# Kernel optimization log

Hardware: AMD Instinct MI355X
Metric: run time of the kernel (lower is better)

## Reference

```python
import jax, jax.numpy as jnp
import numpy as np

NUM_HEADS = 16

def setup_inputs() -> dict:
    key = jax.random.key(0)
    ks = jax.random.split(key, 5)
    N, T, D = 16, 4096, 1024
    # Linear weights stored as (in, out): y = x @ W + b (equivalent to torch x @ W.T + b)
    return {
        "x": jax.random.normal(ks[0], (N, T, D), jnp.float32),
        "w_qkv": jax.random.normal(ks[1], (D, 3 * D), jnp.float32) * (D ** -0.5),
        "b_qkv": jax.random.normal(ks[2], (3 * D,), jnp.float32) * 0.02,
        "w_proj": jax.random.normal(ks[3], (D, D), jnp.float32) * (D ** -0.5),
        "b_proj": jax.random.normal(ks[4], (D,), jnp.float32) * 0.02,
    }

def reference(x, w_qkv, b_qkv, w_proj, b_proj):
    N, T, D = x.shape
    H = NUM_HEADS
    hd = D // H
    scale = hd ** -0.5
    qkv = x @ w_qkv + b_qkv                      # (N,T,3D)
    qkv = qkv.reshape(N, T, 3, H, hd)
    q, k, v = qkv[:, :, 0], qkv[:, :, 1], qkv[:, :, 2]   # each (N,T,H,hd)
    # Faithful to source: matmul over last two dims -> scores across HEADS, (N,T,H,H)
    attn = jnp.einsum('nthd,ntgd->nthg', q * scale, k)
    attn = jax.nn.softmax(attn, axis=-1)
    out = jnp.einsum('nthg,ntgd->nthd', attn, v)         # (N,T,H,hd)
    # Faithful: transpose(2,1) then flatten -> (N,H,T,hd).reshape(N,T,D)
    out = out.transpose(0, 2, 1, 3).reshape(N, T, D)
    return out @ w_proj + b_proj
```

## Files before the change

kernel.cpp:

```cpp
#include <hip/hip_runtime.h>
#include <hip/hip_bf16.h>
#include <stdint.h>

typedef __bf16 bf16x8 __attribute__((ext_vector_type(8)));
typedef float f32x4 __attribute__((ext_vector_type(4)));
typedef unsigned short us8 __attribute__((ext_vector_type(8)));

__device__ __forceinline__ float bf2f(unsigned short u) {
    return __uint_as_float(((unsigned)u) << 16);
}
__device__ __forceinline__ unsigned short f2bf(float f) {
    __bf16 b = (__bf16)f;
    return __builtin_bit_cast(unsigned short, b);
}

__device__ __forceinline__ void gload16(const char* g, char* l) {
    __builtin_amdgcn_global_load_lds(
        (const __attribute__((address_space(1))) void*)g,
        (__attribute__((address_space(3))) void*)l, 16, 0, 0);
}

__global__ __launch_bounds__(256) void transpose_cast(
    const float* __restrict__ in, unsigned short* __restrict__ out,
    int K, int N)
{
    __shared__ float tile[32][33];
    const int tx = threadIdx.x, ty = threadIdx.y;
    const int n0 = blockIdx.x * 32, k0 = blockIdx.y * 32;
    #pragma unroll
    for (int i = 0; i < 32; i += 8)
        tile[ty + i][tx] = in[(long)(k0 + ty + i) * N + n0 + tx];
    __syncthreads();
    #pragma unroll
    for (int i = 0; i < 32; i += 8)
        out[(long)(n0 + ty + i) * K + k0 + tx] = f2bf(tile[tx][ty + i]);
}

__global__ __launch_bounds__(256) void cast_f32_bf16(
    const float* __restrict__ in, unsigned short* __restrict__ out, long n)
{
    const long stride = (long)gridDim.x * 256 * 8;
    for (long i = ((long)blockIdx.x * 256 + threadIdx.x) * 8; i < n; i += stride) {
        const f32x4 u0 = *(const f32x4*)&in[i];
        const f32x4 u1 = *(const f32x4*)&in[i + 4];
        us8 w;
        #pragma unroll
        for (int e = 0; e < 4; ++e) { w[e] = f2bf(u0[e]); w[e + 4] = f2bf(u1[e]); }
        *(us8*)&out[i] = w;
    }
}

#define MFMA16x16(a, b, c) __builtin_amdgcn_mfma_f32_16x16x32_bf16(a, b, c, 0, 0, 0)
#define BAR __builtin_amdgcn_s_barrier()
#define SB  __builtin_amdgcn_sched_barrier(0)
#define P1_ __builtin_amdgcn_s_setprio(1);
#define P0_ __builtin_amdgcn_s_setprio(0);

#define MFMA_H(AA, BB, RO, CO)                                                 \
    _Pragma("unroll") for (int mi_ = 0; mi_ < 4; ++mi_)                        \
        _Pragma("unroll") for (int ni_ = 0; ni_ < 2; ++ni_)                    \
            acc[(RO)+mi_][(CO)+ni_] =                                          \
                MFMA16x16(AA[mi_], BB[ni_], acc[(RO)+mi_][(CO)+ni_]);

#define RD_A(DST, BUFOFF, HIOFF, KS)                                           \
    _Pragma("unroll") for (int mi_ = 0; mi_ < 4; ++mi_)                        \
        DST[mi_] = *(const bf16x8*)(smem + (BUFOFF) + aBase + (HIOFF) + mi_*2048 + (KS));

#define RD_B(DST, BUFOFF, NOFF, KS)                                            \
    _Pragma("unroll") for (int ni_ = 0; ni_ < 2; ++ni_)                        \
        DST[ni_] = *(const bf16x8*)(smem + (BUFOFF) + bBase + ((NOFF)+ni_)*2048 + (KS));

#define TILE8(T_, BUF, OBUF, SG, SR)                                           \
  do {                                                                         \
    const long gk = (long)((T_) + 2) * 128;                                    \
                                                 \
    RD_A(AH0, BUF, 8192, k0)                                                   \
    SB; asm volatile("s_waitcnt lgkmcnt(4)"); SB;                              \
    P1_ MFMA_H(AL0, BL0, 0, 0) P0_                                             \
                                                 \
    RD_B(BH0, BUF, 2, k0)                                                      \
    SB; asm volatile("s_waitcnt lgkmcnt(2)"); SB;                              \
    P1_ MFMA_H(AH0, BL0, 4, 0) P0_                                             \
                                                 \
    RD_A(AL1, BUF, 0, k1)                                                      \
    SB; asm volatile("s_waitcnt lgkmcnt(4)"); SB;                              \
    P1_ MFMA_H(AH0, BH0, 4, 2) P0_                                             \
                                  \
    BAR; RD_B(BL1, BUF, 0, k1)                                                 \
    if (SG) {                                                                  \
        gload16(aStage + (long)(0*64)*Kb + gk, smem + (BUF) + 0*8192 + ldsW);  \
        gload16(aStage + (long)(2*64)*Kb + gk, smem + (BUF) + 2*8192 + ldsW);  \
    }                                                                          \
    SB; asm volatile("s_waitcnt lgkmcnt(2)"); SB;                              \
    P1_ MFMA_H(AL0, BH0, 0, 2) P0_                                             \
                                                 \
    RD_A(AH1, BUF, 8192, k1)                                                   \
    SB; asm volatile("s_waitcnt lgkmcnt(4)"); SB;                              \
    P1_ MFMA_H(AL1, BL1, 0, 0) P0_                                             \
                   \
    BAR; RD_B(BH1, BUF, 2, k1)                                                 \
    if (SG) {                                                                  \
        gload16(aStage + (long)(1*64)*Kb + gk, smem + (BUF) + 1*8192 + ldsW);  \
        gload16(aStage + (long)(3*64)*Kb + gk, smem + (BUF) + 3*8192 + ldsW);  \
    }                                                                          \
    SB; asm volatile("s_waitcnt lgkmcnt(2)"); SB;                              \
    P1_ MFMA_H(AH1, BL1, 4, 0) P0_                                             \
    SB;                                                                        \
    if (SG) asm volatile("s_waitcnt vmcnt(4)");                                \
    else    asm volatile("s_waitcnt vmcnt(0)");                                \
    SB;                                                                        \
                           \
    BAR;                                                                       \
    if (SR) { RD_B(BL0, OBUF, 0, k0) }                                         \
    if (SG) {                                                                  \
        gload16(bStage + (long)(0*64)*Kb + gk, smem + (BUF) + 32768 + 0*8192 + ldsW); \
        gload16(bStage + (long)(1*64)*Kb + gk, smem + (BUF) + 32768 + 1*8192 + ldsW); \
    }                                                                          \
    SB;                                                                        \
    if (SR) asm volatile("s_waitcnt lgkmcnt(2)");                              \
    else    asm volatile("s_waitcnt lgkmcnt(0)");                              \
    SB;                                                                        \
    P1_ MFMA_H(AH1, BH1, 4, 2) P0_                                             \
                           \
    BAR;                                                                       \
    if (SR) { RD_A(AL0, OBUF, 0, k0) }                                         \
    if (SG) {                                                                  \
        gload16(bStage + (long)(2*64)*Kb + gk, smem + (BUF) + 32768 + 2*8192 + ldsW); \
        gload16(bStage + (long)(3*64)*Kb + gk, smem + (BUF) + 32768 + 3*8192 + ldsW); \
    }                                                                          \
    SB;                                                                        \
    if (SR) asm volatile("s_waitcnt lgkmcnt(4)");                              \
    else    asm volatile("s_waitcnt lgkmcnt(0)");                              \
    SB;                                                                        \
    P1_ MFMA_H(AL1, BH1, 0, 2) P0_                                             \
  } while (0)

template<bool OUT_BF16>
__global__ __launch_bounds__(512, 2)
void gemm256(const unsigned short* __restrict__ A,
             const unsigned short* __restrict__ BT,
             const float* __restrict__ bias,
             void* __restrict__ Cp,
             int M, int N, int K)
{
    extern __shared__ char smem[];
    const int tid  = threadIdx.x;
    const int lane = tid & 63;
    const int w    = tid >> 6;
    const int wm   = w >> 2;
    const int wn   = w & 3;

    const int nwg  = gridDim.x;
    const int bid0 = blockIdx.x;
    const int bid  = (bid0 & 7) * (nwg >> 3) + (bid0 >> 3);
    const int nbx  = N >> 8;
    const int bx   = bid % nbx, by = bid / nbx;
    const long rowStart = (long)by * 256;
    const int  colStart = bx * 256;

    const long Kb = (long)K * 2;

    const int srow = w * 8 + (lane >> 3);
    const int scol = ((lane & 7) ^ (lane >> 3)) << 4;
    const char* aStage = (const char*)A  + (rowStart + srow) * Kb + scol;
    const char* bStage = (const char*)BT + ((long)colStart + srow) * Kb + scol;
    const int ldsW = w * 1024;

    const int fr = lane & 15;
    const int kq = lane >> 4;
    const int sw = (fr & 7) << 4;
    const int k0 = (kq * 16) ^ sw;
    const int k1 = (64 + kq * 16) ^ sw;
    const int aBase = (wm * 128 + fr) * 128;
    const int bBase = 32768 + (wn * 64 + fr) * 128;

    f32x4 acc[8][4] = {};
    bf16x8 AL0[4], AH0[4], AL1[4], AH1[4], BL0[2], BH0[2], BL1[2], BH1[2];

    #pragma unroll
    for (int tt = 0; tt < 2; ++tt) {
        #pragma unroll
        for (int j = 0; j < 4; ++j)
            gload16(aStage + (long)(j * 64) * Kb + (long)tt * 128,
                    smem + tt * 65536 + j * 8192 + ldsW);
        #pragma unroll
        for (int j = 0; j < 4; ++j)
            gload16(bStage + (long)(j * 64) * Kb + (long)tt * 128,
                    smem + tt * 65536 + 32768 + j * 8192 + ldsW);
    }
    asm volatile("s_waitcnt vmcnt(8)");
    BAR;
    RD_B(BL0, 0, 0, k0)
    RD_A(AL0, 0, 0, k0)

    #pragma unroll 1
    for (int tp = 0; tp < 7; ++tp) {
        TILE8(2 * tp,     0,     65536, 1, 1);
        TILE8(2 * tp + 1, 65536, 0,     1, 1);
    }
    TILE8(14, 0,     65536, 0, 1);
    TILE8(15, 65536, 0,     0, 0);

    float bv[4];
    #pragma unroll
    for (int ni = 0; ni < 4; ++ni)
        bv[ni] = bias[colStart + wn * 64 + ni * 16 + fr];
    #pragma unroll
    for (int mi = 0; mi < 8; ++mi) {
        #pragma unroll
        for (int ni = 0; ni < 4; ++ni) {
            const int col = colStart + wn * 64 + ni * 16 + fr;
            #pragma unroll
            for (int e = 0; e < 4; ++e) {
                const long row = rowStart + wm * 128 + mi * 16 + kq * 4 + e;
                const float val = acc[mi][ni][e] + bv[ni];
                if constexpr (OUT_BF16)
                    ((unsigned short*)Cp)[row * N + col] = f2bf(val);
                else
                    ((float*)Cp)[row * N + col] = val;
            }
        }
    }
}

__global__ __launch_bounds__(256) void attn_kernel(
    const unsigned short* __restrict__ qkv, unsigned short* __restrict__ out)
{
    __shared__ unsigned short qkvs[4][3072];
    __shared__ float ps[4][320];
    __shared__ unsigned short os[4][1024];
    const int tid = threadIdx.x, lane = tid & 63, wave = tid >> 6;
    const long blockTok = (long)blockIdx.x * 4;

    const unsigned short* src = qkv + blockTok * 3072;
    unsigned short* dstBase = &qkvs[0][0];
    #pragma unroll
    for (int i = 0; i < 6; ++i) {
        const int o = (i * 256 + tid) * 8;
        *(us8*)&dstBase[o] = *(const us8*)&src[o];
    }
    __syncthreads();

    const unsigned short* q  = &qkvs[wave][0];
    const unsigned short* kk = &qkvs[wave][1024];
    const unsigned short* vv = &qkvs[wave][2048];

    const int fr = lane & 15, kq = lane >> 4;
    const int fo = fr * 64 + kq * 8;
    const bf16x8 aq0 = *(const bf16x8*)&q[fo];
    const bf16x8 aq1 = *(const bf16x8*)&q[fo + 32];
    const bf16x8 bk0 = *(const bf16x8*)&kk[fo];
    const bf16x8 bk1 = *(const bf16x8*)&kk[fo + 32];
    f32x4 s = {};
    s = __builtin_amdgcn_mfma_f32_16x16x32_bf16(aq0, bk0, s, 0, 0, 0);
    s = __builtin_amdgcn_mfma_f32_16x16x32_bf16(aq1, bk1, s, 0, 0, 0);

    #pragma unroll
    for (int r = 0; r < 4; ++r) {
        const float v_ = s[r] * 0.125f;
        float m_ = v_;
        m_ = fmaxf(m_, __shfl_xor(m_, 1, 64));
        m_ = fmaxf(m_, __shfl_xor(m_, 2, 64));
        m_ = fmaxf(m_, __shfl_xor(m_, 4, 64));
        m_ = fmaxf(m_, __shfl_xor(m_, 8, 64));
        const float p_ = expf(v_ - m_);
        float t_ = p_;
        t_ += __shfl_xor(t_, 1, 64);
        t_ += __shfl_xor(t_, 2, 64);
        t_ += __shfl_xor(t_, 4, 64);
        t_ += __shfl_xor(t_, 8, 64);
        ps[wave][(kq * 4 + r) * 20 + fr] = p_ / t_;
    }
    __syncthreads();

    const int h = lane >> 2, db = lane & 3;
    float o16[16] = {};
    #pragma unroll
    for (int gq = 0; gq < 4; ++gq) {
        const f32x4 pv = *(const f32x4*)&ps[wave][h * 20 + gq * 4];
        #pragma unroll
        for (int j = 0; j < 4; ++j) {
            const float pg = pv[j];
            const int g = gq * 4 + j;
            const us8 v8a = *(const us8*)&vv[g * 64 + db * 16];
            const us8 v8b = *(const us8*)&vv[g * 64 + db * 16 + 8];
            #pragma unroll
            for (int e = 0; e < 8; ++e) {
                o16[e]     += pg * bf2f(v8a[e]);
                o16[8 + e] += pg * bf2f(v8b[e]);
            }
        }
    }
    us8 w0, w1;
    #pragma unroll
    for (int e = 0; e < 8; ++e) { w0[e] = f2bf(o16[e]); w1[e] = f2bf(o16[8 + e]); }
    *(us8*)&os[wave][h * 64 + db * 16] = w0;
    *(us8*)&os[wave][h * 64 + db * 16 + 8] = w1;
    __syncthreads();

    #pragma unroll
    for (int i = 0; i < 2; ++i) {
        const int c = i * 256 + tid;
        const int w2 = c >> 7;
        const int cc = c & 127;
        const long m = blockTok + w2;
        const long n_ = m >> 12;
        const int t = (int)(m & 4095);
        const int hh = cc >> 3, slot = cc & 7;
        const long row = n_ * 4096 + hh * 256 + (t >> 4);
        const long colb = (long)(t & 15) * 128 + slot * 16;
        *(us8*)((char*)out + row * 2048 + colb) = *(const us8*)&os[w2][cc * 8];
    }
}

extern "C" void kernel_launch(void* const* d_in, const int* in_sizes, int n_in,
                              void* d_out, int out_size, void* d_ws, size_t ws_size,
                              hipStream_t stream) {
    const float* x      = (const float*)d_in[0];
    const float* w_qkv  = (const float*)d_in[1];
    const float* b_qkv  = (const float*)d_in[2];
    const float* w_proj = (const float*)d_in[3];
    const float* b_proj = (const float*)d_in[4];

    const long M = 65536;
    const size_t QKV_B = (size_t)M * 3072 * 2;
    const size_t XB_B  = (size_t)M * 1024 * 2;
    const size_t WQ_B  = 3072 * 1024 * 2;
    const size_t WP_B  = 1024 * 1024 * 2;
    if (ws_size < QKV_B + XB_B + WQ_B + WP_B) return;

    char* ws = (char*)d_ws;
    unsigned short* qkv    = (unsigned short*)ws;
    unsigned short* xb     = (unsigned short*)(ws + QKV_B);
    unsigned short* wqkvT  = (unsigned short*)(ws + QKV_B + XB_B);
    unsigned short* wprojT = (unsigned short*)(ws + QKV_B + XB_B + WQ_B);

    hipFuncSetAttribute((const void*)gemm256<true>,
                        hipFuncAttributeMaxDynamicSharedMemorySize, 131072);
    hipFuncSetAttribute((const void*)gemm256<false>,
                        hipFuncAttributeMaxDynamicSharedMemorySize, 131072);

    dim3 tb(32, 8);
    transpose_cast<<<dim3(3072 / 32, 1024 / 32), tb, 0, stream>>>(w_qkv, wqkvT, 1024, 3072);
    transpose_cast<<<dim3(1024 / 32, 1024 / 32), tb, 0, stream>>>(w_proj, wprojT, 1024, 1024);
    cast_f32_bf16<<<2048, 256, 0, stream>>>(x, xb, M * 1024);

    gemm256<true><<<dim3((3072 / 256) * (M / 256)), 512, 131072, stream>>>(
        xb, wqkvT, b_qkv, qkv, (int)M, 3072, 1024);

    attn_kernel<<<dim3(M / 4), 256, 0, stream>>>(qkv, xb);

    gemm256<false><<<dim3((1024 / 256) * (M / 256)), 512, 131072, stream>>>(
        xb, wprojT, b_proj, d_out, (int)M, 1024, 1024);
}
```

Baseline: 718.5 us.

## Restructure GEMM k-loop into four 16-MFMA phases with full-width B fragments

Replaces the eight-phase tile schedule, where each phase ran 8 MFMAs on half-width B fragments, with a four-phase schedule that runs 16 MFMAs per phase using all four B fragments at once. LDS reads and global-to-LDS staging loads are regrouped into larger batches, and the number of barriers per k-tile drops from four to two. The intent is to cut barrier and waitcnt overhead and give longer uninterrupted MFMA runs. In exchange, fewer LDS reads overlap with compute, and the larger batched loads may stall the MFMA pipe more.

Result: slower. 739.5 us (+2.9%).

```diff
diff --git a/kernel.cpp b/kernel.cpp
--- a/kernel.cpp
+++ b/kernel.cpp
@@ -56,83 +56,61 @@
 #define P1_ __builtin_amdgcn_s_setprio(1);
 #define P0_ __builtin_amdgcn_s_setprio(0);
 
-#define MFMA_H(AA, BB, RO, CO)                                                 \
+#define MFMA16(AA, BB, RO)                                                     \
     _Pragma("unroll") for (int mi_ = 0; mi_ < 4; ++mi_)                        \
-        _Pragma("unroll") for (int ni_ = 0; ni_ < 2; ++ni_)                    \
-            acc[(RO)+mi_][(CO)+ni_] =                                          \
-                MFMA16x16(AA[mi_], BB[ni_], acc[(RO)+mi_][(CO)+ni_]);
-
-#define RD_A(DST, BUFOFF, HIOFF, KS)                                           \
+        _Pragma("unroll") for (int ni_ = 0; ni_ < 4; ++ni_)                    \
+            acc[(RO)+mi_][ni_] =                                               \
+                MFMA16x16(AA[mi_], BB[ni_], acc[(RO)+mi_][ni_]);
+
+#define RD_A4(DST, BUFOFF, HIOFF, KS)                                          \
     _Pragma("unroll") for (int mi_ = 0; mi_ < 4; ++mi_)                        \
         DST[mi_] = *(const bf16x8*)(smem + (BUFOFF) + aBase + (HIOFF) + mi_*2048 + (KS));
 
-#define RD_B(DST, BUFOFF, NOFF, KS)                                            \
-    _Pragma("unroll") for (int ni_ = 0; ni_ < 2; ++ni_)                        \
-        DST[ni_] = *(const bf16x8*)(smem + (BUFOFF) + bBase + ((NOFF)+ni_)*2048 + (KS));
-
-#define TILE8(T_, BUF, OBUF, SG, SR)                                           \
+#define RD_B4(DST, BUFOFF, KS)                                                 \
+    _Pragma("unroll") for (int ni_ = 0; ni_ < 4; ++ni_)                        \
+        DST[ni_] = *(const bf16x8*)(smem + (BUFOFF) + bBase + ni_*2048 + (KS));
+
+#define TILE4(T_, BUF, OBUF, SG, SR)                                           \
   do {                                                                         \
     const long gk = (long)((T_) + 2) * 128;                                    \
-                                                 \
-    RD_A(AH0, BUF, 8192, k0)                                                   \
+                          \
+    RD_A4(AH0, BUF, 8192, k0)                                                  \
     SB; asm volatile("s_waitcnt lgkmcnt(4)"); SB;                              \
-    P1_ MFMA_H(AL0, BL0, 0, 0) P0_                                             \
-                                                 \
-    RD_B(BH0, BUF, 2, k0)                                                      \
-    SB; asm volatile("s_waitcnt lgkmcnt(2)"); SB;                              \
-    P1_ MFMA_H(AH0, BL0, 4, 0) P0_                                             \
-                                                 \
-    RD_A(AL1, BUF, 0, k1)                                                      \
-    SB; asm volatile("s_waitcnt lgkmcnt(4)"); SB;                              \
-    P1_ MFMA_H(AH0, BH0, 4, 2) P0_                                             \
-                                  \
-    BAR; RD_B(BL1, BUF, 0, k1)                                                 \
+    P1_ MFMA16(AL0, B0, 0) P0_                                                 \
+                                           \
+    RD_A4(AL1, BUF, 0, k1)                                                     \
+    RD_B4(B1, BUF, k1)                                                         \
+    SB; asm volatile("s_waitcnt lgkmcnt(8)"); SB;                              \
+    P1_ MFMA16(AH0, B0, 4) P0_                                                 \
+           \
+    BAR;                                                                       \
+    RD_A4(AH1, BUF, 8192, k1)                                                  \
     if (SG) {                                                                  \
         gload16(aStage + (long)(0*64)*Kb + gk, smem + (BUF) + 0*8192 + ldsW);  \
         gload16(aStage + (long)(2*64)*Kb + gk, smem + (BUF) + 2*8192 + ldsW);  \
+        gload16(bStage + (long)(0*64)*Kb + gk, smem + (BUF) + 32768 + 0*8192 + ldsW); \
+        gload16(bStage + (long)(1*64)*Kb + gk, smem + (BUF) + 32768 + 1*8192 + ldsW); \
     }                                                                          \
-    SB; asm volatile("s_waitcnt lgkmcnt(2)"); SB;                              \
-    P1_ MFMA_H(AL0, BH0, 0, 2) P0_                                             \
-                                                 \
-    RD_A(AH1, BUF, 8192, k1)                                                   \
     SB; asm volatile("s_waitcnt lgkmcnt(4)"); SB;                              \
-    P1_ MFMA_H(AL1, BL1, 0, 0) P0_                                             \
-                   \
-    BAR; RD_B(BH1, BUF, 2, k1)                                                 \
-    if (SG) {                                                                  \
-        gload16(aStage + (long)(1*64)*Kb + gk, smem + (BUF) + 1*8192 + ldsW);  \
-        gload16(aStage + (long)(3*64)*Kb + gk, smem + (BUF) + 3*8192 + ldsW);  \
-    }                                                                          \
-    SB; asm volatile("s_waitcnt lgkmcnt(2)"); SB;                              \
-    P1_ MFMA_H(AH1, BL1, 4, 0) P0_                                             \
+    P1_ MFMA16(AL1, B1, 0) P0_                                                 \
     SB;                                                                        \
     if (SG) asm volatile("s_waitcnt vmcnt(4)");                                \
     else    asm volatile("s_waitcnt vmcnt(0)");                                \
     SB;                                                                        \
-                           \
+      \
     BAR;                                                                       \
-    if (SR) { RD_B(BL0, OBUF, 0, k0) }                                         \
+    if (SR) { RD_A4(AL0, OBUF, 0, k0) RD_B4(B0, OBUF, k0) }                    \
     if (SG) {                                                                  \
-        gload16(bStage + (long)(0*64)*Kb + gk, smem + (BUF) + 32768 + 0*8192 + ldsW); \
-        gload16(bStage + (long)(1*64)*Kb + gk, smem + (BUF) + 32768 + 1*8192 + ldsW); \
-    }                                                                          \
-    SB;                                                                        \
-    if (SR) asm volatile("s_waitcnt lgkmcnt(2)");                              \
-    else    asm volatile("s_waitcnt lgkmcnt(0)");                              \
-    SB;                                                                        \
-    P1_ MFMA_H(AH1, BH1, 4, 2) P0_                                             \
-                           \
-    BAR;                                                                       \
-    if (SR) { RD_A(AL0, OBUF, 0, k0) }                                         \
-    if (SG) {                                                                  \
+        gload16(aStage + (long)(1*64)*Kb + gk, smem + (BUF) + 1*8192 + ldsW);  \
+        gload16(aStage + (long)(3*64)*Kb + gk, smem + (BUF) + 3*8192 + ldsW);  \
         gload16(bStage + (long)(2*64)*Kb + gk, smem + (BUF) + 32768 + 2*8192 + ldsW); \
         gload16(bStage + (long)(3*64)*Kb + gk, smem + (BUF) + 32768 + 3*8192 + ldsW); \
     }                                                                          \
     SB;                                                                        \
-    if (SR) asm volatile("s_waitcnt lgkmcnt(4)");                              \
+    if (SR) asm volatile("s_waitcnt lgkmcnt(8)");                              \
     else    asm volatile("s_waitcnt lgkmcnt(0)");                              \
     SB;                                                                        \
-    P1_ MFMA_H(AL1, BH1, 0, 2) P0_                                             \
+    P1_ MFMA16(AH1, B1, 4) P0_                                                 \
   } while (0)
 
 template<bool OUT_BF16>
@@ -175,7 +153,7 @@
     const int bBase = 32768 + (wn * 64 + fr) * 128;
 
     f32x4 acc[8][4] = {};
-    bf16x8 AL0[4], AH0[4], AL1[4], AH1[4], BL0[2], BH0[2], BL1[2], BH1[2];
+    bf16x8 AL0[4], AH0[4], AL1[4], AH1[4], B0[4], B1[4];
 
     #pragma unroll
     for (int tt = 0; tt < 2; ++tt) {
@@ -190,16 +168,16 @@
     }
     asm volatile("s_waitcnt vmcnt(8)");
     BAR;
-    RD_B(BL0, 0, 0, k0)
-    RD_A(AL0, 0, 0, k0)
+    RD_B4(B0, 0, k0)
+    RD_A4(AL0, 0, 0, k0)
 
     #pragma unroll 1
     for (int tp = 0; tp < 7; ++tp) {
-        TILE8(2 * tp,     0,     65536, 1, 1);
-        TILE8(2 * tp + 1, 65536, 0,     1, 1);
-    }
-    TILE8(14, 0,     65536, 0, 1);
-    TILE8(15, 65536, 0,     0, 0);
+        TILE4(2 * tp,     0,     65536, 1, 1);
+        TILE4(2 * tp + 1, 65536, 0,     1, 1);
+    }
+    TILE4(14, 0,     65536, 0, 1);
+    TILE4(15, 65536, 0,     0, 0);
 
     float bv[4];
     #pragma unroll
```
